# Kernel tuning notes

Measured on AMD Instinct MI355X. Metric: run time of the kernel, lower is better.

Reference implementation:

```python
import jax, jax.numpy as jnp
import numpy as np

EPS = 1e-8

def _ste(x, q):
    # straight-through estimator: forward = q, backward = identity
    return x + jax.lax.stop_gradient(q - x)

def quant_act_uint8(x):
    # per-tensor uint8 activation fake-quant (Brevitas Uint8ActPerTensorFloat style)
    s = jax.lax.stop_gradient(jnp.maximum(jnp.max(x), EPS)) / 255.0
    q = jnp.clip(jnp.round(x / s), 0.0, 255.0) * s
    return _ste(x, q), s

def quant_weight_int8_perchannel(w):
    # per-output-channel symmetric int8 fake-quant; w: [out, in]
    s = jax.lax.stop_gradient(jnp.maximum(jnp.max(jnp.abs(w), axis=1, keepdims=True), EPS)) / 127.0
    q = jnp.clip(jnp.round(w / s), -128.0, 127.0) * s
    return _ste(w, q), s[:, 0]

def quant_bias_int32(b, s_in, s_w):
    # bias quantized at scale s_in * s_w[c] (Brevitas Int32Bias)
    s = jax.lax.stop_gradient(s_in * s_w)
    q = jnp.round(b / s) * s
    return _ste(b, q)

def quant_linear(x, w, b):
    xq, s_in = quant_act_uint8(x)
    wq, s_w = quant_weight_int8_perchannel(w)
    bq = quant_bias_int32(b, s_in, s_w)
    return jnp.einsum('btd,fd->btf', xq, wq) + bq

def setup_inputs() -> dict:
    key = jax.random.key(0)
    k1, k2, k3, k4, k5 = jax.random.split(key, 5)
    B, S, D, F = 4, 2048, 1024, 4096
    return {
        'x': jax.random.normal(k1, (B, S, D), dtype=jnp.float32),
        'w1': jax.random.normal(k2, (F, D), dtype=jnp.float32) * (1.0 / np.sqrt(D)),
        'b1': jax.random.normal(k3, (F,), dtype=jnp.float32) * 0.01,
        'w2': jax.random.normal(k4, (D, F), dtype=jnp.float32) * (1.0 / np.sqrt(F)),
        'b2': jax.random.normal(k5, (D,), dtype=jnp.float32) * 0.01,
    }

def reference(x, w1, b1, w2, b2):
    h = jax.nn.relu(quant_linear(x, w1, b1))
    # dropout is identity in eval mode
    return quant_linear(h, w2, b2)
```

## Files before the change

kernel.cpp:

```cpp
#include <hip/hip_runtime.h>
#include <stdint.h>

#define EPSQ 1e-8f

typedef __attribute__((ext_vector_type(4))) int i32x4;

__device__ __forceinline__ unsigned enc_f(float f) {
    unsigned u = __float_as_uint(f);
    return (u & 0x80000000u) ? ~u : (u | 0x80000000u);
}
__device__ __forceinline__ float dec_f(unsigned u) {
    return (u & 0x80000000u) ? __uint_as_float(u & 0x7fffffffu)
                             : __uint_as_float(~u);
}

__device__ __forceinline__ float wave_max_f(float v) {
    #pragma unroll
    for (int off = 32; off; off >>= 1) v = fmaxf(v, __shfl_xor(v, off));
    return v;
}
__device__ __forceinline__ int wave_sum_i(int v) {
    #pragma unroll
    for (int off = 32; off; off >>= 1) v += __shfl_xor(v, off);
    return v;
}

__global__ __launch_bounds__(256) void k_prep(
    const float4* __restrict__ x, long n4x, float* __restrict__ partials,
    const float* __restrict__ w1, signed char* __restrict__ w1q,
    float* __restrict__ sw1, int* __restrict__ rs1,
    const float* __restrict__ w2, signed char* __restrict__ w2q,
    float* __restrict__ sw2, int* __restrict__ rs2) {
    __shared__ float sm[4];
    __shared__ int   si[4];
    int b = blockIdx.x;
    int wid = threadIdx.x >> 6;
    if (b < 2048) {
        long i = (long)b * 256 + threadIdx.x;
        float m = -3.4e38f;
        for (; i < n4x; i += 2048L * 256) {
            float4 v = x[i];
            m = fmaxf(fmaxf(m, fmaxf(v.x, v.y)), fmaxf(v.z, v.w));
        }
        m = wave_max_f(m);
        if ((threadIdx.x & 63) == 0) sm[wid] = m;
        __syncthreads();
        if (threadIdx.x == 0)
            partials[b] = fmaxf(fmaxf(sm[0], sm[1]), fmaxf(sm[2], sm[3]));
        return;
    }
    const float* w; signed char* q; float* s_out; int* rs_out; int row, L;
    if (b < 2048 + 4096) { row = b - 2048; w = w1; q = w1q; s_out = sw1; rs_out = rs1; L = 1024; }
    else                 { row = b - 6144; w = w2; q = w2q; s_out = sw2; rs_out = rs2; L = 4096; }

    const float4* wr = (const float4*)(w + (long)row * L);
    int n4 = L >> 2;
    float m = 0.0f;
    for (int i = threadIdx.x; i < n4; i += 256) {
        float4 v = wr[i];
        m = fmaxf(m, fmaxf(fmaxf(fabsf(v.x), fabsf(v.y)),
                           fmaxf(fabsf(v.z), fabsf(v.w))));
    }
    m = wave_max_f(m);
    if ((threadIdx.x & 63) == 0) sm[wid] = m;
    __syncthreads();
    m = fmaxf(fmaxf(sm[0], sm[1]), fmaxf(sm[2], sm[3]));
    float s = fmaxf(m, EPSQ) / 127.0f;

    char4* qr = (char4*)(q + (long)row * L);
    int isum = 0;
    for (int i = threadIdx.x; i < n4; i += 256) {
        float4 v = wr[i];
        int a = min(max((int)rintf(v.x / s), -128), 127);
        int bb = min(max((int)rintf(v.y / s), -128), 127);
        int c = min(max((int)rintf(v.z / s), -128), 127);
        int d = min(max((int)rintf(v.w / s), -128), 127);
        isum += a + bb + c + d;
        char4 cc; cc.x = (char)a; cc.y = (char)bb; cc.z = (char)c; cc.w = (char)d;
        qr[i] = cc;
    }
    isum = wave_sum_i(isum);
    if ((threadIdx.x & 63) == 0) si[wid] = isum;
    __syncthreads();
    if (threadIdx.x == 0) {
        s_out[row]  = s;
        rs_out[row] = si[0] + si[1] + si[2] + si[3];
    }
}

__global__ __launch_bounds__(256) void k_reduce_max(const float* __restrict__ partials,
                                                    int n, unsigned* __restrict__ slot) {
    __shared__ float sm[4];
    float m = -3.4e38f;
    for (int i = threadIdx.x; i < n; i += 256) m = fmaxf(m, partials[i]);
    m = wave_max_f(m);
    if ((threadIdx.x & 63) == 0) sm[threadIdx.x >> 6] = m;
    __syncthreads();
    if (threadIdx.x == 0)
        *slot = enc_f(fmaxf(fmaxf(sm[0], sm[1]), fmaxf(sm[2], sm[3])));
}

__global__ __launch_bounds__(256) void k_quant_act(const float4* __restrict__ in,
                                                   char4* __restrict__ out, long n4,
                                                   const unsigned* __restrict__ slot) {
    float s = fmaxf(dec_f(*slot), EPSQ) / 255.0f;
    long i = (long)blockIdx.x * 256 + threadIdx.x;
    for (; i < n4; i += (long)gridDim.x * 256) {
        float4 v = in[i];
        int a = min(max((int)rintf(v.x / s), 0), 255) - 128;
        int b = min(max((int)rintf(v.y / s), 0), 255) - 128;
        int c = min(max((int)rintf(v.z / s), 0), 255) - 128;
        int d = min(max((int)rintf(v.w / s), 0), 255) - 128;
        char4 cc; cc.x = (char)a; cc.y = (char)b; cc.z = (char)c; cc.w = (char)d;
        out[i] = cc;
    }
}

__device__ __forceinline__ void gl_lds16(const signed char* g, signed char* l) {
    __builtin_amdgcn_global_load_lds(
        (const __attribute__((address_space(1))) unsigned int*)g,
        (__attribute__((address_space(3))) unsigned int*)l, 16, 0, 0);
}

template<int MODE>
__global__ __launch_bounds__(256, 3) void k_gemm_i8(
    const signed char* __restrict__ A,
    const signed char* __restrict__ B,
    const float* __restrict__ s_w,
    const int* __restrict__ rowsum,
    const float* __restrict__ bias,
    const unsigned* __restrict__ act_slot,
    float* __restrict__ Cf,
    signed char* __restrict__ Cq,
    unsigned* __restrict__ omax_slot,
    int M, int N, long K) {
    __shared__ __align__(16) signed char Als[16384];
    __shared__ __align__(16) signed char Bls[16384];
    __shared__ float red[4];

    const int t    = threadIdx.x;
    const int lane = t & 63;
    const int w    = t >> 6;
    const int m0   = blockIdx.y * 128;
    const int n0   = blockIdx.x * 128;
    const int mr   = lane & 15;
    const int qq   = lane >> 4;

    const signed char* a0 = A + (long)(m0 + w * 32 + mr) * K + qq * 16;
    const signed char* b0 = B + (long)(n0 + w * 32 + mr) * K + qq * 16;
    signed char* ad = Als + w * 4096 + lane * 16;
    signed char* bd = Bls + w * 4096 + lane * 16;

    const int wrow = (w >> 1) * 64;
    const int wcol = (w & 1) * 64;
    const int a_base = (w >> 1) * 8192 + lane * 16;
    const int b_base = (w & 1) * 8192 + lane * 16;

    i32x4 acc[4][4];
    #pragma unroll
    for (int i = 0; i < 4; i++)
        #pragma unroll
        for (int j = 0; j < 4; j++) acc[i][j] = (i32x4){0, 0, 0, 0};

    for (long k0 = 0; k0 < K; k0 += 128) {
        __syncthreads();
        gl_lds16(a0 + k0,               ad);
        gl_lds16(a0 + k0 + 64,          ad + 1024);
        gl_lds16(a0 + k0 + 16 * K,      ad + 2048);
        gl_lds16(a0 + k0 + 16 * K + 64, ad + 3072);
        gl_lds16(b0 + k0,               bd);
        gl_lds16(b0 + k0 + 64,          bd + 1024);
        gl_lds16(b0 + k0 + 16 * K,      bd + 2048);
        gl_lds16(b0 + k0 + 16 * K + 64, bd + 3072);
        __syncthreads();

        #pragma unroll
        for (int kk = 0; kk < 2; kk++) {
            i32x4 af[4], bf[4];
            #pragma unroll
            for (int i = 0; i < 4; i++)
                af[i] = *(const i32x4*)(Als + a_base + i * 2048 + kk * 1024);
            #pragma unroll
            for (int j = 0; j < 4; j++)
                bf[j] = *(const i32x4*)(Bls + b_base + j * 2048 + kk * 1024);
            #pragma unroll
            for (int i = 0; i < 4; i++)
                #pragma unroll
                for (int j = 0; j < 4; j++)
                    acc[i][j] = __builtin_amdgcn_mfma_i32_16x16x64_i8(
                        af[i], bf[j], acc[i][j], 0, 0, 0);
        }
    }

    const float s_act = fmaxf(dec_f(*act_slot), EPSQ) / 255.0f;

    if (MODE == 1) {
        float lmax = 0.0f;
        #pragma unroll
        for (int j = 0; j < 4; j++) {
            int im = -2147483647 - 1;
            #pragma unroll
            for (int i = 0; i < 4; i++)
                #pragma unroll
                for (int r = 0; r < 4; r++) im = max(im, acc[i][j][r]);
            int gn = n0 + wcol + j * 16 + mr;
            float ssc  = s_act * s_w[gn];
            float bint = rintf(bias[gn] / ssc);
            float h = ssc * ((float)(im + 128 * rowsum[gn]) + bint);
            lmax = fmaxf(lmax, h);
        }
        lmax = fmaxf(lmax, 0.0f);
        lmax = wave_max_f(lmax);
        if (lane == 0) red[w] = lmax;
        __syncthreads();
        if (t == 0)
            atomicMax(omax_slot,
                      enc_f(fmaxf(fmaxf(red[0], red[1]), fmaxf(red[2], red[3]))));
        return;
    }

    float s_oq = 1.0f;
    if (MODE == 2) s_oq = fmaxf(dec_f(*omax_slot), EPSQ) / 255.0f;

    #pragma unroll
    for (int j = 0; j < 4; j++) {
        int gn = n0 + wcol + j * 16 + mr;
        float ssc  = s_act * s_w[gn];
        float bint = rintf(bias[gn] / ssc);
        int   icor = 128 * rowsum[gn];
        float fq   = (MODE == 2) ? (ssc / s_oq) : 0.0f;
        #pragma unroll
        for (int i = 0; i < 4; i++) {
            #pragma unroll
            for (int r = 0; r < 4; r++) {
                int gm = m0 + wrow + i * 16 + qq * 4 + r;
                float v = (float)(acc[i][j][r] + icor) + bint;
                if (MODE == 0) {
                    Cf[(long)gm * N + gn] = ssc * v;
                } else {
                    int qv = min(max((int)rintf(fq * v), 0), 255) - 128;
                    Cq[(long)gm * N + gn] = (signed char)qv;
                }
            }
        }
    }
}

extern "C" void kernel_launch(void* const* d_in, const int* in_sizes, int n_in,
                              void* d_out, int out_size, void* d_ws, size_t ws_size,
                              hipStream_t stream) {
    const float* x  = (const float*)d_in[0];
    const float* w1 = (const float*)d_in[1];
    const float* b1 = (const float*)d_in[2];
    const float* w2 = (const float*)d_in[3];
    const float* b2 = (const float*)d_in[4];
    float* out = (float*)d_out;

    const int M = 8192, D = 1024, F = 4096;

    char* ws = (char*)d_ws;
    size_t off = 0;
    unsigned* slots = (unsigned*)ws;               off += 256;
    float* partials = (float*)(ws + off);          off += 2048 * 4;
    signed char* xi  = (signed char*)(ws + off);   off += (size_t)M * D;
    signed char* w1q = (signed char*)(ws + off);   off += (size_t)F * D;
    signed char* w2q = (signed char*)(ws + off);   off += (size_t)D * F;
    float* sw1 = (float*)(ws + off);               off += (size_t)F * 4;
    float* sw2 = (float*)(ws + off);               off += (size_t)D * 4;
    int* rs1   = (int*)(ws + off);                 off += (size_t)F * 4;
    int* rs2   = (int*)(ws + off);                 off += (size_t)D * 4;
    signed char* hq = (signed char*)(ws + off);    off += (size_t)M * F;

    hipMemsetAsync(slots, 0, 8, stream);

    k_prep<<<dim3(2048 + F + D), dim3(256), 0, stream>>>(
        (const float4*)x, (long)M * D / 4, partials,
        w1, w1q, sw1, rs1, w2, w2q, sw2, rs2);
    k_reduce_max<<<dim3(1), dim3(256), 0, stream>>>(partials, 2048, slots + 0);
    k_quant_act<<<dim3(2048), dim3(256), 0, stream>>>((const float4*)x, (char4*)xi,
                                                      (long)M * D / 4, slots + 0);
    k_gemm_i8<1><<<dim3(F / 128, M / 128), dim3(256), 0, stream>>>(
        xi, w1q, sw1, rs1, b1, slots + 0, nullptr, nullptr, slots + 1, M, F, (long)D);
    k_gemm_i8<2><<<dim3(F / 128, M / 128), dim3(256), 0, stream>>>(
        xi, w1q, sw1, rs1, b1, slots + 0, nullptr, hq, slots + 1, M, F, (long)D);
    k_gemm_i8<0><<<dim3(D / 128, M / 128), dim3(256), 0, stream>>>(
        hq, w2q, sw2, rs2, b2, slots + 1, out, nullptr, nullptr, M, D, (long)F);

    (void)in_sizes; (void)n_in; (void)out_size; (void)ws_size;
}
```

Baseline: 318.5 us.

## Switch int8 GEMM to 32x32x32 MFMA tiles with matching LDS layout

Replaces the 4x4 grid of 16x16x64 int8 MFMAs per wave with a 2x2 grid of 32x32x32 MFMAs, changing the global-to-LDS load pattern, fragment reads and epilogue row mapping to match. The larger MFMA shape cuts the number of LDS fragment loads per K step and the instruction count. Launch bounds are raised from 3 to 4 blocks per CU to improve occupancy. The trade-offs are more register pressure under the tighter launch bound and a different output write pattern in the epilogue.

```diff
diff --git a/kernel.cpp b/kernel.cpp
--- a/kernel.cpp
+++ b/kernel.cpp
@@ -3,7 +3,8 @@
 
 #define EPSQ 1e-8f
 
-typedef __attribute__((ext_vector_type(4))) int i32x4;
+typedef __attribute__((ext_vector_type(4)))  int i32x4;
+typedef __attribute__((ext_vector_type(16))) int i32x16;
 
 __device__ __forceinline__ unsigned enc_f(float f) {
     unsigned u = __float_as_uint(f);
@@ -123,7 +124,7 @@
 }
 
 template<int MODE>
-__global__ __launch_bounds__(256, 3) void k_gemm_i8(
+__global__ __launch_bounds__(256, 4) void k_gemm_i8(
     const signed char* __restrict__ A,
     const signed char* __restrict__ B,
     const float* __restrict__ s_w,
@@ -143,11 +144,11 @@
     const int w    = t >> 6;
     const int m0   = blockIdx.y * 128;
     const int n0   = blockIdx.x * 128;
-    const int mr   = lane & 15;
-    const int qq   = lane >> 4;
-
-    const signed char* a0 = A + (long)(m0 + w * 32 + mr) * K + qq * 16;
-    const signed char* b0 = B + (long)(n0 + w * 32 + mr) * K + qq * 16;
+    const int lr   = lane & 31;
+    const int lh   = lane >> 5;
+
+    const signed char* a0 = A + (long)(m0 + w * 32 + lr) * K + lh * 16;
+    const signed char* b0 = B + (long)(n0 + w * 32 + lr) * K + lh * 16;
     signed char* ad = Als + w * 4096 + lane * 16;
     signed char* bd = Bls + w * 4096 + lane * 16;
 
@@ -156,38 +157,37 @@
     const int a_base = (w >> 1) * 8192 + lane * 16;
     const int b_base = (w & 1) * 8192 + lane * 16;
 
-    i32x4 acc[4][4];
-    #pragma unroll
-    for (int i = 0; i < 4; i++)
-        #pragma unroll
-        for (int j = 0; j < 4; j++) acc[i][j] = (i32x4){0, 0, 0, 0};
+    i32x16 acc[2][2];
+    #pragma unroll
+    for (int i = 0; i < 2; i++)
+        #pragma unroll
+        for (int j = 0; j < 2; j++)
+            #pragma unroll
+            for (int r = 0; r < 16; r++) acc[i][j][r] = 0;
 
     for (long k0 = 0; k0 < K; k0 += 128) {
         __syncthreads();
-        gl_lds16(a0 + k0,               ad);
-        gl_lds16(a0 + k0 + 64,          ad + 1024);
-        gl_lds16(a0 + k0 + 16 * K,      ad + 2048);
-        gl_lds16(a0 + k0 + 16 * K + 64, ad + 3072);
-        gl_lds16(b0 + k0,               bd);
-        gl_lds16(b0 + k0 + 64,          bd + 1024);
-        gl_lds16(b0 + k0 + 16 * K,      bd + 2048);
-        gl_lds16(b0 + k0 + 16 * K + 64, bd + 3072);
-        __syncthreads();
-
-        #pragma unroll
-        for (int kk = 0; kk < 2; kk++) {
-            i32x4 af[4], bf[4];
-            #pragma unroll
-            for (int i = 0; i < 4; i++)
-                af[i] = *(const i32x4*)(Als + a_base + i * 2048 + kk * 1024);
-            #pragma unroll
-            for (int j = 0; j < 4; j++)
-                bf[j] = *(const i32x4*)(Bls + b_base + j * 2048 + kk * 1024);
-            #pragma unroll
-            for (int i = 0; i < 4; i++)
+        #pragma unroll
+        for (int q = 0; q < 4; q++) {
+            gl_lds16(a0 + k0 + q * 32, ad + q * 1024);
+            gl_lds16(b0 + k0 + q * 32, bd + q * 1024);
+        }
+        __syncthreads();
+
+        #pragma unroll
+        for (int q = 0; q < 4; q++) {
+            i32x4 af[2], bf[2];
+            #pragma unroll
+            for (int i = 0; i < 2; i++)
+                af[i] = *(const i32x4*)(Als + a_base + i * 4096 + q * 1024);
+            #pragma unroll
+            for (int j = 0; j < 2; j++)
+                bf[j] = *(const i32x4*)(Bls + b_base + j * 4096 + q * 1024);
+            #pragma unroll
+            for (int i = 0; i < 2; i++)
                 #pragma unroll
-                for (int j = 0; j < 4; j++)
-                    acc[i][j] = __builtin_amdgcn_mfma_i32_16x16x64_i8(
+                for (int j = 0; j < 2; j++)
+                    acc[i][j] = __builtin_amdgcn_mfma_i32_32x32x32_i8(
                         af[i], bf[j], acc[i][j], 0, 0, 0);
         }
     }
@@ -197,13 +197,13 @@
     if (MODE == 1) {
         float lmax = 0.0f;
         #pragma unroll
-        for (int j = 0; j < 4; j++) {
+        for (int j = 0; j < 2; j++) {
             int im = -2147483647 - 1;
             #pragma unroll
-            for (int i = 0; i < 4; i++)
+            for (int i = 0; i < 2; i++)
                 #pragma unroll
-                for (int r = 0; r < 4; r++) im = max(im, acc[i][j][r]);
-            int gn = n0 + wcol + j * 16 + mr;
+                for (int r = 0; r < 16; r++) im = max(im, acc[i][j][r]);
+            int gn = n0 + wcol + j * 32 + lr;
             float ssc  = s_act * s_w[gn];
             float bint = rintf(bias[gn] / ssc);
             float h = ssc * ((float)(im + 128 * rowsum[gn]) + bint);
@@ -223,17 +223,17 @@
     if (MODE == 2) s_oq = fmaxf(dec_f(*omax_slot), EPSQ) / 255.0f;
 
     #pragma unroll
-    for (int j = 0; j < 4; j++) {
-        int gn = n0 + wcol + j * 16 + mr;
+    for (int j = 0; j < 2; j++) {
+        int gn = n0 + wcol + j * 32 + lr;
         float ssc  = s_act * s_w[gn];
         float bint = rintf(bias[gn] / ssc);
         int   icor = 128 * rowsum[gn];
         float fq   = (MODE == 2) ? (ssc / s_oq) : 0.0f;
         #pragma unroll
-        for (int i = 0; i < 4; i++) {
-            #pragma unroll
-            for (int r = 0; r < 4; r++) {
-                int gm = m0 + wrow + i * 16 + qq * 4 + r;
+        for (int i = 0; i < 2; i++) {
+            #pragma unroll
+            for (int r = 0; r < 16; r++) {
+                int gm = m0 + wrow + i * 32 + (r & 3) + 8 * (r >> 2) + 4 * lh;
                 float v = (float)(acc[i][j][r] + icor) + bint;
                 if (MODE == 0) {
                     Cf[(long)gm * N + gn] = ssc * v;
```

Result: slower. 342.5 us (+7.5%).

## Double-buffer A tiles in LDS and load B fragments directly from global

Applied to the files above, without the earlier changes.

Turns the A-tile staging into a two-buffer pipeline: the next K-slice is fetched into LDS while the current one is consumed, leaving one barrier per iteration. B is no longer staged through LDS; each wave reads its B fragments straight from global memory into registers. The aim is to overlap global loads with MFMA work and cut LDS traffic and synchronisation. In exchange, B is now read once per wave pair instead of once per block, which raises global/L2 traffic, and the direct global loads may stall the MFMAs if their latency is not hidden.

```diff
diff --git a/kernel.cpp b/kernel.cpp
--- a/kernel.cpp
+++ b/kernel.cpp
@@ -134,8 +134,7 @@
     signed char* __restrict__ Cq,
     unsigned* __restrict__ omax_slot,
     int M, int N, long K) {
-    __shared__ __align__(16) signed char Als[16384];
-    __shared__ __align__(16) signed char Bls[16384];
+    __shared__ __align__(16) signed char Als[2][16384];
     __shared__ float red[4];
 
     const int t    = threadIdx.x;
@@ -147,14 +146,13 @@
     const int qq   = lane >> 4;
 
     const signed char* a0 = A + (long)(m0 + w * 32 + mr) * K + qq * 16;
-    const signed char* b0 = B + (long)(n0 + w * 32 + mr) * K + qq * 16;
-    signed char* ad = Als + w * 4096 + lane * 16;
-    signed char* bd = Bls + w * 4096 + lane * 16;
+    const int ad_off = w * 4096 + lane * 16;
 
     const int wrow = (w >> 1) * 64;
     const int wcol = (w & 1) * 64;
     const int a_base = (w >> 1) * 8192 + lane * 16;
-    const int b_base = (w & 1) * 8192 + lane * 16;
+
+    const signed char* bbase = B + (long)(n0 + wcol + mr) * K + qq * 16;
 
     i32x4 acc[4][4];
     #pragma unroll
@@ -162,33 +160,42 @@
         #pragma unroll
         for (int j = 0; j < 4; j++) acc[i][j] = (i32x4){0, 0, 0, 0};
 
-    for (long k0 = 0; k0 < K; k0 += 128) {
+    auto stage_A = [&](signed char* buf, long k0) {
+        gl_lds16(a0 + k0,               buf + ad_off);
+        gl_lds16(a0 + k0 + 64,          buf + ad_off + 1024);
+        gl_lds16(a0 + k0 + 16 * K,      buf + ad_off + 2048);
+        gl_lds16(a0 + k0 + 16 * K + 64, buf + ad_off + 3072);
+    };
+
+    const int NIT = (int)(K >> 7);
+    stage_A(Als[0], 0);
+
+    for (int it = 0; it < NIT; ++it) {
+        const int cur = it & 1;
+        __builtin_amdgcn_s_waitcnt(0x0F70);
         __syncthreads();
-        gl_lds16(a0 + k0,               ad);
-        gl_lds16(a0 + k0 + 64,          ad + 1024);
-        gl_lds16(a0 + k0 + 16 * K,      ad + 2048);
-        gl_lds16(a0 + k0 + 16 * K + 64, ad + 3072);
-        gl_lds16(b0 + k0,               bd);
-        gl_lds16(b0 + k0 + 64,          bd + 1024);
-        gl_lds16(b0 + k0 + 16 * K,      bd + 2048);
-        gl_lds16(b0 + k0 + 16 * K + 64, bd + 3072);
-        __syncthreads();
-
+        if (it + 1 < NIT)
+            stage_A(Als[cur ^ 1], (long)(it + 1) * 128);
+
+        i32x4 bf[2][4];
+        #pragma unroll
+        for (int kk = 0; kk < 2; kk++)
+            #pragma unroll
+            for (int j = 0; j < 4; j++)
+                bf[kk][j] = *(const i32x4*)(bbase + (long)j * 16 * K
+                                            + (long)it * 128 + kk * 64);
         #pragma unroll
         for (int kk = 0; kk < 2; kk++) {
-            i32x4 af[4], bf[4];
+            i32x4 af[4];
             #pragma unroll
             for (int i = 0; i < 4; i++)
-                af[i] = *(const i32x4*)(Als + a_base + i * 2048 + kk * 1024);
-            #pragma unroll
-            for (int j = 0; j < 4; j++)
-                bf[j] = *(const i32x4*)(Bls + b_base + j * 2048 + kk * 1024);
+                af[i] = *(const i32x4*)(Als[cur] + a_base + i * 2048 + kk * 1024);
             #pragma unroll
             for (int i = 0; i < 4; i++)
                 #pragma unroll
                 for (int j = 0; j < 4; j++)
                     acc[i][j] = __builtin_amdgcn_mfma_i32_16x16x64_i8(
-                        af[i], bf[j], acc[i][j], 0, 0, 0);
+                        af[i], bf[kk][j], acc[i][j], 0, 0, 0);
         }
     }
 
```

After: 400.1 us. 25.6% more time.
